# Optimization experiments

Measured on AMD Instinct MI355X. Metric: run time of the kernel, lower is better.

Reference implementation:

```python
import jax, jax.numpy as jnp
import numpy as np

N = 8192
E = 262144
D_IN = 768
D_STRUCT = 32
D_HID = 768
D_OUT = 768
MEM_K = 64
MEM_D = 768
NUM_GRAPHS = 64


def setup_inputs() -> dict:
    key = jax.random.key(0)
    ks = jax.random.split(key, 16)
    s = 0.02
    return {
        "feature": jax.random.normal(ks[0], (N, D_IN), jnp.float32),
        "ppr": jax.random.uniform(ks[1], (N,), jnp.float32),
        "edge_attr": jax.random.normal(ks[2], (E, D_IN), jnp.float32),
        "Ws": jax.random.normal(ks[3], (1, D_STRUCT), jnp.float32) * s,
        "bs": jnp.zeros((D_STRUCT,), jnp.float32),
        "W1": jax.random.normal(ks[4], (D_IN + D_STRUCT, D_HID), jnp.float32) * s,
        "b1": jnp.zeros((D_HID,), jnp.float32),
        "prelu_a": jnp.asarray(0.25, jnp.float32),
        "W2": jax.random.normal(ks[5], (D_HID, D_OUT), jnp.float32) * s,
        "b2": jnp.zeros((D_OUT,), jnp.float32),
        "Wp1": jax.random.normal(ks[6], (D_HID, D_HID), jnp.float32) * s,
        "bp1": jnp.zeros((D_HID,), jnp.float32),
        "Wp2": jax.random.normal(ks[7], (D_HID, D_OUT), jnp.float32) * s,
        "bp2": jnp.zeros((D_OUT,), jnp.float32),
        "memory": jax.random.normal(ks[8], (MEM_K, MEM_D), jnp.float32),
        "edge_index": jax.random.randint(ks[9], (2, E), 0, N, jnp.int64),
        "batch_ids": jnp.sort(jax.random.randint(ks[10], (N,), 0, NUM_GRAPHS, jnp.int64)),
        "num_graphs": NUM_GRAPHS,
    }


def reference(feature, ppr, edge_attr, Ws, bs, W1, b1, prelu_a, W2, b2,
              Wp1, bp1, Wp2, bp2, memory, edge_index, batch_ids, num_graphs):
    n = feature.shape[0]
    # aggre_edges: scatter_add edge_attr onto destination nodes (col)
    col = edge_index[1]
    feat = feature + jax.ops.segment_sum(edge_attr, col, num_segments=n)
    # struct encoder: Linear(1, struct_dim) + ReLU on ppr scalar
    struct_feat = jax.nn.relu(ppr[:, None] @ Ws + bs)  # [N, 32]
    # MLP: Linear -> PReLU -> Linear
    h = jnp.concatenate([feat, struct_feat], axis=-1) @ W1 + b1
    h = jnp.where(h > 0, h, prelu_a * h)
    node_feats = h @ W2 + b2  # [N, D_OUT]
    # scatter_mean over graphs
    seg_sum = jax.ops.segment_sum(node_feats, batch_ids, num_segments=num_graphs)
    cnt = jax.ops.segment_sum(jnp.ones((n,), node_feats.dtype), batch_ids, num_segments=num_graphs)
    graph_feats = seg_sum / jnp.maximum(cnt, 1.0)[:, None]
    pooled_feats = jnp.tanh(graph_feats @ Wp1 + bp1) @ Wp2 + bp2
    # memory attention: softmax(M @ nf) over memory slots, then mean(mem_key * M)
    # mean_k(softmax(scores)[n,k] * M[k,d]) == (softmax @ M) / K
    w = jax.nn.softmax(node_feats @ memory.T, axis=1)  # [N, 64]
    re_node_feats = (w @ memory) / memory.shape[0]      # [N, 768]
    loss = jnp.mean((node_feats - re_node_feats) ** 2)
    return pooled_feats, re_node_feats, loss
```

## Files before the change

kernel.cpp:

```cpp
#include <hip/hip_runtime.h>
#include <hip/hip_bf16.h>
#include <math.h>

typedef unsigned short ushort_t;
typedef short bf16x8 __attribute__((ext_vector_type(8)));
typedef float f32x4 __attribute__((ext_vector_type(4)));

#define NNODES   8192
#define DIN      768
#define DSTRUCT  32
#define XDIM     800
#define DHID     768
#define DOUT     768
#define MEMK     64
#define NGRAPH   64
#define BUCKET_CAP 128

#define OFF_XHI     0u
#define OFF_XLO     (OFF_XHI  + 8192u*800u*2u)
#define OFF_HHI     (OFF_XLO  + 8192u*800u*2u)
#define OFF_HLO     (OFF_HHI  + 8192u*768u*2u)
#define OFF_NF      (OFF_HLO  + 8192u*768u*2u)
#define OFF_NFHI    (OFF_NF   + 8192u*768u*4u)
#define OFF_NFLO    (OFF_NFHI + 8192u*768u*2u)
#define OFF_W1THI   (OFF_NFLO + 8192u*768u*2u)
#define OFF_W1TLO   (OFF_W1THI + 768u*800u*2u)
#define OFF_W2THI   (OFF_W1TLO + 768u*800u*2u)
#define OFF_W2TLO   (OFF_W2THI + 768u*768u*2u)
#define OFF_MHI     (OFF_W2TLO + 768u*768u*2u)
#define OFF_MLO     (OFF_MHI  + 64u*768u*2u)
#define OFF_MTHI    (OFF_MLO  + 64u*768u*2u)
#define OFF_MTLO    (OFF_MTHI + 768u*64u*2u)
#define OFF_BUCKET  (OFF_MTLO + 768u*64u*2u)
#define OFF_COUNTS  (OFF_BUCKET + 8192u*BUCKET_CAP*4u)
#define OFF_GSTART  (OFF_COUNTS + 8192u*4u)
#define OFF_GEND    (OFF_GSTART + 256u)
#define OFF_LOSS    (OFF_GEND + 256u)
#define OFF_GFEAT   (OFF_LOSS + 256u)
#define OFF_T1      (OFF_GFEAT + 768u*64u*4u)
#define ZERO_OFF    OFF_COUNTS
#define ZERO_BYTES  (8192u*4u + 256u + 256u + 256u)

__device__ __forceinline__ ushort_t bf_rne(float f) {
    unsigned u = __float_as_uint(f);
    return (ushort_t)((u + 0x7FFFu + ((u >> 16) & 1u)) >> 16);
}
__device__ __forceinline__ void split_bf16(float f, ushort_t& hi, ushort_t& lo) {
    ushort_t h = bf_rne(f);
    float fh = __uint_as_float(((unsigned)h) << 16);
    hi = h;
    lo = bf_rne(f - fh);
}
__device__ __forceinline__ void gld16(const void* g, void* l) {
    __builtin_amdgcn_global_load_lds(
        (const __attribute__((address_space(1))) unsigned int*)g,
        (__attribute__((address_space(3))) unsigned int*)l, 16, 0, 0);
}

__global__ void k_fill_bucket(const int* __restrict__ col, int* __restrict__ counts,
                              int* __restrict__ bucket, int E) {
    for (int e = blockIdx.x * blockDim.x + threadIdx.x; e < E; e += gridDim.x * blockDim.x) {
        int c = col[e];
        if ((unsigned)c < (unsigned)NNODES) {
            int p = atomicAdd(&counts[c], 1);
            if (p < BUCKET_CAP) bucket[c * BUCKET_CAP + p] = e;
        }
    }
}

__global__ __launch_bounds__(192) void k_aggregate(
    const float* __restrict__ feature, const float* __restrict__ edge_attr,
    const float* __restrict__ ppr, const float* __restrict__ Ws, const float* __restrict__ bs,
    const int* __restrict__ bucket, const int* __restrict__ counts,
    ushort_t* __restrict__ Xhi, ushort_t* __restrict__ Xlo) {
    int n = blockIdx.x;
    int t = threadIdx.x;
    const float4* frow = (const float4*)(feature + (size_t)n * DIN);
    float4 acc = frow[t];
    int deg = min(counts[n], BUCKET_CAP);
    const int* bk = bucket + n * BUCKET_CAP;
    for (int j = 0; j < deg; ++j) {
        int e = bk[j];
        float4 v = ((const float4*)(edge_attr + (size_t)e * DIN))[t];
        acc.x += v.x; acc.y += v.y; acc.z += v.z; acc.w += v.w;
    }
    ushort4 h4, l4;
    split_bf16(acc.x, h4.x, l4.x); split_bf16(acc.y, h4.y, l4.y);
    split_bf16(acc.z, h4.z, l4.z); split_bf16(acc.w, h4.w, l4.w);
    *(ushort4*)(Xhi + (size_t)n * XDIM + t * 4) = h4;
    *(ushort4*)(Xlo + (size_t)n * XDIM + t * 4) = l4;
    if (t < DSTRUCT / 4) {
        float p = ppr[n];
        int k = t * 4;
        float4 s;
        s.x = fmaxf(p * Ws[k+0] + bs[k+0], 0.f);
        s.y = fmaxf(p * Ws[k+1] + bs[k+1], 0.f);
        s.z = fmaxf(p * Ws[k+2] + bs[k+2], 0.f);
        s.w = fmaxf(p * Ws[k+3] + bs[k+3], 0.f);
        ushort4 sh, sl;
        split_bf16(s.x, sh.x, sl.x); split_bf16(s.y, sh.y, sl.y);
        split_bf16(s.z, sh.z, sl.z); split_bf16(s.w, sh.w, sl.w);
        *(ushort4*)(Xhi + (size_t)n * XDIM + DIN + k) = sh;
        *(ushort4*)(Xlo + (size_t)n * XDIM + DIN + k) = sl;
    }
}

__global__ __launch_bounds__(256) void k_wsplit(const float* __restrict__ W,
                                                ushort_t* __restrict__ Thi, ushort_t* __restrict__ Tlo,
                                                int K, int N) {
    __shared__ float tile[32][33];
    int n0 = blockIdx.x * 32, k0 = blockIdx.y * 32;
    int tx = threadIdx.x & 31, ty = threadIdx.x >> 5;
#pragma unroll
    for (int i = 0; i < 4; ++i) {
        int k = ty + i * 8;
        tile[k][tx] = W[(size_t)(k0 + k) * N + n0 + tx];
    }
    __syncthreads();
#pragma unroll
    for (int i = 0; i < 4; ++i) {
        int nn = ty + i * 8;
        float v = tile[tx][nn];
        ushort_t hi, lo; split_bf16(v, hi, lo);
        Thi[(size_t)(n0 + nn) * K + k0 + tx] = hi;
        Tlo[(size_t)(n0 + nn) * K + k0 + tx] = lo;
    }
}

__global__ void k_msplit(const float* __restrict__ m, ushort_t* __restrict__ hi,
                         ushort_t* __restrict__ lo, int n) {
    int i = blockIdx.x * 256 + threadIdx.x;
    if (i >= n) return;
    ushort_t h, l; split_bf16(m[i], h, l);
    hi[i] = h; lo[i] = l;
}

#define L_ALO 2048
#define L_BHI 4096
#define L_BLO 8192
#define L_BUF 12288

template<int ACT, int OUTMODE>
__global__ __launch_bounds__(256) void k_gemm_mfma(
    const ushort_t* __restrict__ Ahi, const ushort_t* __restrict__ Alo,
    const ushort_t* __restrict__ Bhi, const ushort_t* __restrict__ Blo,
    const float* __restrict__ bias, const float* __restrict__ act_p,
    float* __restrict__ Cf, ushort_t* __restrict__ Chi, ushort_t* __restrict__ Clo,
    int M, int N, int K) {
    __shared__ ushort_t lds[2 * L_BUF];
    int tid = threadIdx.x;
    int l = tid & 63, w = tid >> 6;

    int nbx = N / 128;
    int nwg = nbx * (M / 64);
    int bid = blockIdx.y * nbx + blockIdx.x;
    int q = nwg >> 3;
    int nb = (bid & 7) * q + (bid >> 3);
    int bx = nb % nbx, by = nb / nbx;
    int m0 = by * 64, n0 = bx * 128;

    int wm = w >> 1, wn = w & 1;

    f32x4 acc[2][4];
#pragma unroll
    for (int m = 0; m < 2; ++m)
#pragma unroll
        for (int n = 0; n < 4; ++n) acc[m][n] = (f32x4){0.f, 0.f, 0.f, 0.f};

    int srow = w * 16 + (l >> 2);
    int sc   = (l & 3) * 8;
    const ushort_t* agh  = Ahi + (size_t)(m0 + srow) * K + sc;
    const ushort_t* agl  = Alo + (size_t)(m0 + srow) * K + sc;
    const ushort_t* bgh0 = Bhi + (size_t)(n0 + srow) * K + sc;
    const ushort_t* bgh1 = Bhi + (size_t)(n0 + 64 + srow) * K + sc;
    const ushort_t* bgl0 = Blo + (size_t)(n0 + srow) * K + sc;
    const ushort_t* bgl1 = Blo + (size_t)(n0 + 64 + srow) * K + sc;

    int NT = K / 32;

    {
        ushort_t* b = lds;
        gld16(agh,  b + w * 512);
        gld16(agl,  b + L_ALO + w * 512);
        gld16(bgh0, b + L_BHI + w * 512);
        gld16(bgh1, b + L_BHI + 2048 + w * 512);
        gld16(bgl0, b + L_BLO + w * 512);
        gld16(bgl1, b + L_BLO + 2048 + w * 512);
    }

    int c0 = l >> 4;
    int arow = wm * 32 + (l & 15);
    int bcol = wn * 64 + (l & 15);

    for (int kt = 0; kt < NT; ++kt) {
        int cur = kt & 1;
        __syncthreads();
        if (kt + 1 < NT) {
            int ko = (kt + 1) * 32;
            ushort_t* b = lds + (cur ^ 1) * L_BUF;
            gld16(agh + ko,  b + w * 512);
            gld16(agl + ko,  b + L_ALO + w * 512);
            gld16(bgh0 + ko, b + L_BHI + w * 512);
            gld16(bgh1 + ko, b + L_BHI + 2048 + w * 512);
            gld16(bgl0 + ko, b + L_BLO + w * 512);
            gld16(bgl1 + ko, b + L_BLO + 2048 + w * 512);
        }
        const ushort_t* cb = lds + cur * L_BUF;
        bf16x8 ah[2], al[2], bh[4], bl[4];
#pragma unroll
        for (int m = 0; m < 2; ++m) {
            ah[m] = *(const bf16x8*)(cb + (arow + m * 16) * 32 + c0 * 8);
            al[m] = *(const bf16x8*)(cb + L_ALO + (arow + m * 16) * 32 + c0 * 8);
        }
#pragma unroll
        for (int n = 0; n < 4; ++n) {
            bh[n] = *(const bf16x8*)(cb + L_BHI + (bcol + n * 16) * 32 + c0 * 8);
            bl[n] = *(const bf16x8*)(cb + L_BLO + (bcol + n * 16) * 32 + c0 * 8);
        }
#pragma unroll
        for (int m = 0; m < 2; ++m)
#pragma unroll
            for (int n = 0; n < 4; ++n) {
                acc[m][n] = __builtin_amdgcn_mfma_f32_16x16x32_bf16(ah[m], bh[n], acc[m][n], 0, 0, 0);
                acc[m][n] = __builtin_amdgcn_mfma_f32_16x16x32_bf16(ah[m], bl[n], acc[m][n], 0, 0, 0);
                acc[m][n] = __builtin_amdgcn_mfma_f32_16x16x32_bf16(al[m], bh[n], acc[m][n], 0, 0, 0);
            }
    }

    float ap = (ACT == 1) ? *act_p : 0.f;
#pragma unroll
    for (int m = 0; m < 2; ++m)
#pragma unroll
        for (int n = 0; n < 4; ++n) {
            int col = n0 + wn * 64 + n * 16 + (l & 15);
            float bv = bias[col];
#pragma unroll
            for (int r = 0; r < 4; ++r) {
                int row = m0 + wm * 32 + m * 16 + (l >> 4) * 4 + r;
                float x = acc[m][n][r] + bv;
                if (ACT == 1) x = x > 0.f ? x : ap * x;
                ushort_t hi, lo; split_bf16(x, hi, lo);
                Chi[(size_t)row * N + col] = hi;
                Clo[(size_t)row * N + col] = lo;
                if (OUTMODE == 2) Cf[(size_t)row * N + col] = x;
            }
        }
}

__global__ void k_boundaries(const int* __restrict__ batch, int* __restrict__ gstart,
                             int* __restrict__ gend, int n) {
    int i = blockIdx.x * blockDim.x + threadIdx.x;
    if (i >= n) return;
    int b = batch[i];
    if ((unsigned)b >= (unsigned)NGRAPH) return;
    if (i == 0 || batch[i - 1] != b) gstart[b] = i;
    if (i == n - 1 || batch[i + 1] != b) gend[b] = i + 1;
}

__global__ __launch_bounds__(128) void k_pool(const float* __restrict__ nf,
                                              const int* __restrict__ gstart, const int* __restrict__ gend,
                                              float* __restrict__ gfeatT) {
    int g = blockIdx.x, d = blockIdx.y * 128 + threadIdx.x;
    int s = gstart[g], e = gend[g];
    float a = 0.f;
    for (int n = s; n < e; ++n) a += nf[(size_t)n * DOUT + d];
    gfeatT[(size_t)d * 64 + g] = a / fmaxf((float)(e - s), 1.f);
}

template<int ACT>
__global__ __launch_bounds__(256) void k_mlp_t(const float* __restrict__ AT, const float* __restrict__ B,
                                               const float* __restrict__ bias,
                                               float* __restrict__ OutT, float* __restrict__ OutR) {
    __shared__ float red[4][64];
    int n = blockIdx.x;
    int l = threadIdx.x & 63, qw = threadIdx.x >> 6;
    float s = 0.f;
    const float* a = AT + l;
    const float* b = B + n;
#pragma unroll 8
    for (int k = qw * 192; k < qw * 192 + 192; ++k)
        s = fmaf(a[k * 64], b[k * 768], s);
    red[qw][l] = s;
    __syncthreads();
    if (threadIdx.x < 64) {
        float v = red[0][l] + red[1][l] + red[2][l] + red[3][l] + bias[n];
        if (ACT == 2) { v = tanhf(v); OutT[n * 64 + l] = v; }
        else OutR[(size_t)l * 768 + n] = v;
    }
}

__global__ __launch_bounds__(256) void k_attn(
    const ushort_t* __restrict__ NFhi, const ushort_t* __restrict__ NFlo,
    const ushort_t* __restrict__ Mhi,  const ushort_t* __restrict__ Mlo,
    const ushort_t* __restrict__ MThi, const ushort_t* __restrict__ MTlo,
    const float* __restrict__ nf, float* __restrict__ re, float* __restrict__ lossac) {
    __shared__ ushort_t Ah[96 * 32 * 8];
    __shared__ ushort_t Al[96 * 32 * 8];
    __shared__ ushort_t Wp[2][32 * 64];
    __shared__ float xch[4][32];
    __shared__ float lred[4];
    int tid = threadIdx.x, l = tid & 63, w = tid >> 6;
    int g = l >> 4, li = l & 15;
    int base = blockIdx.x * 32;

    for (int i = w * 12; i < w * 12 + 12; ++i) {
        int kc = i * 2 + (l >> 5), row = l & 31;
        gld16(NFhi + (size_t)(base + row) * 768 + kc * 8, Ah + i * 512);
        gld16(NFlo + (size_t)(base + row) * 768 + kc * 8, Al + i * 512);
    }
    __syncthreads();

    f32x4 sacc[2];
    sacc[0] = (f32x4){0.f,0.f,0.f,0.f}; sacc[1] = (f32x4){0.f,0.f,0.f,0.f};
    int slot = w * 16 + li;
#pragma unroll 4
    for (int kt = 0; kt < 24; ++kt) {
        bf16x8 ah0 = *(const bf16x8*)(Ah + (kt * 4 + g) * 256 + li * 8);
        bf16x8 ah1 = *(const bf16x8*)(Ah + (kt * 4 + g) * 256 + (li + 16) * 8);
        bf16x8 al0 = *(const bf16x8*)(Al + (kt * 4 + g) * 256 + li * 8);
        bf16x8 al1 = *(const bf16x8*)(Al + (kt * 4 + g) * 256 + (li + 16) * 8);
        bf16x8 bh  = *(const bf16x8*)(Mhi + (size_t)slot * 768 + kt * 32 + g * 8);
        bf16x8 bl  = *(const bf16x8*)(Mlo + (size_t)slot * 768 + kt * 32 + g * 8);
        sacc[0] = __builtin_amdgcn_mfma_f32_16x16x32_bf16(ah0, bh, sacc[0], 0, 0, 0);
        sacc[0] = __builtin_amdgcn_mfma_f32_16x16x32_bf16(ah0, bl, sacc[0], 0, 0, 0);
        sacc[0] = __builtin_amdgcn_mfma_f32_16x16x32_bf16(al0, bh, sacc[0], 0, 0, 0);
        sacc[1] = __builtin_amdgcn_mfma_f32_16x16x32_bf16(ah1, bh, sacc[1], 0, 0, 0);
        sacc[1] = __builtin_amdgcn_mfma_f32_16x16x32_bf16(ah1, bl, sacc[1], 0, 0, 0);
        sacc[1] = __builtin_amdgcn_mfma_f32_16x16x32_bf16(al1, bh, sacc[1], 0, 0, 0);
    }

    float mxv[8];
#pragma unroll
    for (int m = 0; m < 2; ++m)
#pragma unroll
        for (int r = 0; r < 4; ++r) {
            float v = sacc[m][r];
            v = fmaxf(v, __shfl_xor(v, 1)); v = fmaxf(v, __shfl_xor(v, 2));
            v = fmaxf(v, __shfl_xor(v, 4)); v = fmaxf(v, __shfl_xor(v, 8));
            mxv[m * 4 + r] = v;
        }
    if (li == 0) {
#pragma unroll
        for (int m = 0; m < 2; ++m)
#pragma unroll
            for (int r = 0; r < 4; ++r) xch[w][m * 16 + g * 4 + r] = mxv[m * 4 + r];
    }
    __syncthreads();
    float ev[8], sv[8];
#pragma unroll
    for (int m = 0; m < 2; ++m)
#pragma unroll
        for (int r = 0; r < 4; ++r) {
            int row = m * 16 + g * 4 + r;
            float mx = fmaxf(fmaxf(xch[0][row], xch[1][row]), fmaxf(xch[2][row], xch[3][row]));
            float e = __expf(sacc[m][r] - mx);
            ev[m * 4 + r] = e;
            float s = e;
            s += __shfl_xor(s, 1); s += __shfl_xor(s, 2);
            s += __shfl_xor(s, 4); s += __shfl_xor(s, 8);
            sv[m * 4 + r] = s;
        }
    __syncthreads();
    if (li == 0) {
#pragma unroll
        for (int m = 0; m < 2; ++m)
#pragma unroll
            for (int r = 0; r < 4; ++r) xch[w][m * 16 + g * 4 + r] = sv[m * 4 + r];
    }
    __syncthreads();
#pragma unroll
    for (int m = 0; m < 2; ++m)
#pragma unroll
        for (int r = 0; r < 4; ++r) {
            int row = m * 16 + g * 4 + r;
            float tot = xch[0][row] + xch[1][row] + xch[2][row] + xch[3][row];
            float wv = ev[m * 4 + r] / tot;
            ushort_t hi, lo; split_bf16(wv, hi, lo);
            int idx = row * 64 + (slot ^ ((row & 7) << 3));
            Wp[0][idx] = hi; Wp[1][idx] = lo;
        }
    __syncthreads();

    bf16x8 wah[2][2], wal[2][2];
#pragma unroll
    for (int m = 0; m < 2; ++m)
#pragma unroll
        for (int kt2 = 0; kt2 < 2; ++kt2) {
            int row = m * 16 + li;
            int k8 = kt2 * 4 + g;
            int idx = row * 64 + ((k8 * 8) ^ ((row & 7) << 3));
            wah[m][kt2] = *(const bf16x8*)&Wp[0][idx];
            wal[m][kt2] = *(const bf16x8*)&Wp[1][idx];
        }
    float lp = 0.f;
#pragma unroll 2
    for (int nfi = 0; nfi < 12; ++nfi) {
        int col = w * 192 + nfi * 16 + li;
        f32x4 pacc[2];
        pacc[0] = (f32x4){0.f,0.f,0.f,0.f}; pacc[1] = (f32x4){0.f,0.f,0.f,0.f};
#pragma unroll
        for (int kt2 = 0; kt2 < 2; ++kt2) {
            bf16x8 bh = *(const bf16x8*)(MThi + (size_t)col * 64 + kt2 * 32 + g * 8);
            bf16x8 bl = *(const bf16x8*)(MTlo + (size_t)col * 64 + kt2 * 32 + g * 8);
#pragma unroll
            for (int m = 0; m < 2; ++m) {
                pacc[m] = __builtin_amdgcn_mfma_f32_16x16x32_bf16(wah[m][kt2], bh, pacc[m], 0, 0, 0);
                pacc[m] = __builtin_amdgcn_mfma_f32_16x16x32_bf16(wah[m][kt2], bl, pacc[m], 0, 0, 0);
                pacc[m] = __builtin_amdgcn_mfma_f32_16x16x32_bf16(wal[m][kt2], bh, pacc[m], 0, 0, 0);
            }
        }
#pragma unroll
        for (int m = 0; m < 2; ++m)
#pragma unroll
            for (int r = 0; r < 4; ++r) {
                int row = base + m * 16 + g * 4 + r;
                float v = pacc[m][r] * (1.f / 64.f);
                float x = nf[(size_t)row * 768 + col];
                re[(size_t)row * 768 + col] = v;
                float d = x - v;
                lp = fmaf(d, d, lp);
            }
    }
    for (int o = 32; o; o >>= 1) lp += __shfl_xor(lp, o);
    if (l == 0) lred[w] = lp;
    __syncthreads();
    if (tid == 0) atomicAdd(lossac, lred[0] + lred[1] + lred[2] + lred[3]);
}

__global__ void k_loss_final(const float* __restrict__ acc, float* __restrict__ out, float invn) {
    if (threadIdx.x == 0 && blockIdx.x == 0) out[0] = acc[0] * invn;
}

extern "C" void kernel_launch(void* const* d_in, const int* in_sizes, int n_in,
                              void* d_out, int out_size, void* d_ws, size_t ws_size,
                              hipStream_t stream) {
    const float* feature  = (const float*)d_in[0];
    const float* ppr      = (const float*)d_in[1];
    const float* edge_attr= (const float*)d_in[2];
    const float* Ws       = (const float*)d_in[3];
    const float* bs       = (const float*)d_in[4];
    const float* W1       = (const float*)d_in[5];
    const float* b1       = (const float*)d_in[6];
    const float* prelu_a  = (const float*)d_in[7];
    const float* W2       = (const float*)d_in[8];
    const float* b2       = (const float*)d_in[9];
    const float* Wp1      = (const float*)d_in[10];
    const float* bp1      = (const float*)d_in[11];
    const float* Wp2      = (const float*)d_in[12];
    const float* bp2      = (const float*)d_in[13];
    const float* memory   = (const float*)d_in[14];
    const int*   edge_index = (const int*)d_in[15];
    const int*   batch_ids  = (const int*)d_in[16];

    const int E = in_sizes[15] / 2;
    const int N = in_sizes[0] / DIN;
    const int* col = edge_index + E;

    char* ws = (char*)d_ws;
    ushort_t* Xhi  = (ushort_t*)(ws + OFF_XHI);
    ushort_t* Xlo  = (ushort_t*)(ws + OFF_XLO);
    ushort_t* Hhi  = (ushort_t*)(ws + OFF_HHI);
    ushort_t* Hlo  = (ushort_t*)(ws + OFF_HLO);
    float*    nf   = (float*)   (ws + OFF_NF);
    ushort_t* NFhi = (ushort_t*)(ws + OFF_NFHI);
    ushort_t* NFlo = (ushort_t*)(ws + OFF_NFLO);
    ushort_t* W1Thi= (ushort_t*)(ws + OFF_W1THI);
    ushort_t* W1Tlo= (ushort_t*)(ws + OFF_W1TLO);
    ushort_t* W2Thi= (ushort_t*)(ws + OFF_W2THI);
    ushort_t* W2Tlo= (ushort_t*)(ws + OFF_W2TLO);
    ushort_t* Mhi  = (ushort_t*)(ws + OFF_MHI);
    ushort_t* Mlo  = (ushort_t*)(ws + OFF_MLO);
    ushort_t* MThi = (ushort_t*)(ws + OFF_MTHI);
    ushort_t* MTlo = (ushort_t*)(ws + OFF_MTLO);
    int*   bucket = (int*)(ws + OFF_BUCKET);
    int*   counts = (int*)(ws + OFF_COUNTS);
    int*   gstart = (int*)(ws + OFF_GSTART);
    int*   gend   = (int*)(ws + OFF_GEND);
    float* lossac = (float*)(ws + OFF_LOSS);
    float* gfeatT = (float*)(ws + OFF_GFEAT);
    float* t1T    = (float*)(ws + OFF_T1);

    float* out_pooled = (float*)d_out;
    float* out_re     = (float*)d_out + NGRAPH * DOUT;
    float* out_loss   = (float*)d_out + NGRAPH * DOUT + (size_t)N * DOUT;

    (void)hipMemsetAsync(ws + ZERO_OFF, 0, ZERO_BYTES, stream);

    k_wsplit<<<dim3(768 / 32, 800 / 32), 256, 0, stream>>>(W1, W1Thi, W1Tlo, XDIM, DHID);
    k_wsplit<<<dim3(768 / 32, 768 / 32), 256, 0, stream>>>(W2, W2Thi, W2Tlo, DHID, DOUT);
    k_wsplit<<<dim3(768 / 32, 64 / 32), 256, 0, stream>>>(memory, MThi, MTlo, MEMK, DOUT);
    k_msplit<<<(MEMK * 768 + 255) / 256, 256, 0, stream>>>(memory, Mhi, Mlo, MEMK * 768);

    k_fill_bucket<<<1024, 256, 0, stream>>>(col, counts, bucket, E);
    k_aggregate<<<N, 192, 0, stream>>>(feature, edge_attr, ppr, Ws, bs, bucket, counts, Xhi, Xlo);

    k_gemm_mfma<1, 1><<<dim3(DHID / 128, N / 64), 256, 0, stream>>>(
        Xhi, Xlo, W1Thi, W1Tlo, b1, prelu_a, nullptr, Hhi, Hlo, N, DHID, XDIM);
    k_gemm_mfma<0, 2><<<dim3(DOUT / 128, N / 64), 256, 0, stream>>>(
        Hhi, Hlo, W2Thi, W2Tlo, b2, nullptr, nf, NFhi, NFlo, N, DOUT, DHID);

    k_boundaries<<<(N + 255) / 256, 256, 0, stream>>>(batch_ids, gstart, gend, N);
    k_pool<<<dim3(NGRAPH, 6), 128, 0, stream>>>(nf, gstart, gend, gfeatT);

    k_mlp_t<2><<<768, 256, 0, stream>>>(gfeatT, Wp1, bp1, t1T, nullptr);
    k_mlp_t<0><<<768, 256, 0, stream>>>(t1T, Wp2, bp2, nullptr, out_pooled);

    k_attn<<<N / 32, 256, 0, stream>>>(NFhi, NFlo, Mhi, Mlo, MThi, MTlo, nf, out_re, lossac);
    k_loss_final<<<1, 64, 0, stream>>>(lossac, out_loss, 1.f / (float)((size_t)N * DOUT));
}
```

Measured before the change: 414.4 us.

## Drop fp32 node-feature buffer and reorganize GEMM LDS tile layout

Removes the fp32 copy of node features written by the second GEMM; the pooling and attention kernels now rebuild each value from its bf16 hi/lo pair. This cuts about 25 MB of global writes and the matching reads. The GEMM's global-to-LDS staging is also remapped so each 16-row block is stored k-chunk-major. That makes the per-lane bf16x8 LDS reads contiguous across lanes and should reduce bank conflicts. The rebuilt value differs slightly from the original fp32 (about 16 mantissa bits), which changes the loss and pooling numerics a little.

```diff
diff --git a/kernel.cpp b/kernel.cpp
--- a/kernel.cpp
+++ b/kernel.cpp
@@ -20,8 +20,7 @@
 #define OFF_XLO     (OFF_XHI  + 8192u*800u*2u)
 #define OFF_HHI     (OFF_XLO  + 8192u*800u*2u)
 #define OFF_HLO     (OFF_HHI  + 8192u*768u*2u)
-#define OFF_NF      (OFF_HLO  + 8192u*768u*2u)
-#define OFF_NFHI    (OFF_NF   + 8192u*768u*4u)
+#define OFF_NFHI    (OFF_HLO  + 8192u*768u*2u)
 #define OFF_NFLO    (OFF_NFHI + 8192u*768u*2u)
 #define OFF_W1THI   (OFF_NFLO + 8192u*768u*2u)
 #define OFF_W1TLO   (OFF_W1THI + 768u*800u*2u)
@@ -51,6 +50,9 @@
     hi = h;
     lo = bf_rne(f - fh);
 }
+__device__ __forceinline__ float join_bf16(ushort_t hi, ushort_t lo) {
+    return __uint_as_float(((unsigned)hi) << 16) + __uint_as_float(((unsigned)lo) << 16);
+}
 __device__ __forceinline__ void gld16(const void* g, void* l) {
     __builtin_amdgcn_global_load_lds(
         (const __attribute__((address_space(1))) unsigned int*)g,
@@ -140,12 +142,12 @@
 #define L_BLO 8192
 #define L_BUF 12288
 
-template<int ACT, int OUTMODE>
+template<int ACT>
 __global__ __launch_bounds__(256) void k_gemm_mfma(
     const ushort_t* __restrict__ Ahi, const ushort_t* __restrict__ Alo,
     const ushort_t* __restrict__ Bhi, const ushort_t* __restrict__ Blo,
     const float* __restrict__ bias, const float* __restrict__ act_p,
-    float* __restrict__ Cf, ushort_t* __restrict__ Chi, ushort_t* __restrict__ Clo,
+    ushort_t* __restrict__ Chi, ushort_t* __restrict__ Clo,
     int M, int N, int K) {
     __shared__ ushort_t lds[2 * L_BUF];
     int tid = threadIdx.x;
@@ -167,8 +169,8 @@
 #pragma unroll
         for (int n = 0; n < 4; ++n) acc[m][n] = (f32x4){0.f, 0.f, 0.f, 0.f};
 
-    int srow = w * 16 + (l >> 2);
-    int sc   = (l & 3) * 8;
+    int srow = w * 16 + (l & 15);
+    int sc   = (l >> 4) * 8;
     const ushort_t* agh  = Ahi + (size_t)(m0 + srow) * K + sc;
     const ushort_t* agl  = Alo + (size_t)(m0 + srow) * K + sc;
     const ushort_t* bgh0 = Bhi + (size_t)(n0 + srow) * K + sc;
@@ -189,8 +191,7 @@
     }
 
     int c0 = l >> 4;
-    int arow = wm * 32 + (l & 15);
-    int bcol = wn * 64 + (l & 15);
+    int li = l & 15;
 
     for (int kt = 0; kt < NT; ++kt) {
         int cur = kt & 1;
@@ -209,13 +210,13 @@
         bf16x8 ah[2], al[2], bh[4], bl[4];
 #pragma unroll
         for (int m = 0; m < 2; ++m) {
-            ah[m] = *(const bf16x8*)(cb + (arow + m * 16) * 32 + c0 * 8);
-            al[m] = *(const bf16x8*)(cb + L_ALO + (arow + m * 16) * 32 + c0 * 8);
+            ah[m] = *(const bf16x8*)(cb + (wm * 2 + m) * 512 + c0 * 128 + li * 8);
+            al[m] = *(const bf16x8*)(cb + L_ALO + (wm * 2 + m) * 512 + c0 * 128 + li * 8);
         }
 #pragma unroll
         for (int n = 0; n < 4; ++n) {
-            bh[n] = *(const bf16x8*)(cb + L_BHI + (bcol + n * 16) * 32 + c0 * 8);
-            bl[n] = *(const bf16x8*)(cb + L_BLO + (bcol + n * 16) * 32 + c0 * 8);
+            bh[n] = *(const bf16x8*)(cb + L_BHI + (wn * 4 + n) * 512 + c0 * 128 + li * 8);
+            bl[n] = *(const bf16x8*)(cb + L_BLO + (wn * 4 + n) * 512 + c0 * 128 + li * 8);
         }
 #pragma unroll
         for (int m = 0; m < 2; ++m)
@@ -242,7 +243,6 @@
                 ushort_t hi, lo; split_bf16(x, hi, lo);
                 Chi[(size_t)row * N + col] = hi;
                 Clo[(size_t)row * N + col] = lo;
-                if (OUTMODE == 2) Cf[(size_t)row * N + col] = x;
             }
         }
 }
@@ -257,13 +257,15 @@
     if (i == n - 1 || batch[i + 1] != b) gend[b] = i + 1;
 }
 
-__global__ __launch_bounds__(128) void k_pool(const float* __restrict__ nf,
+__global__ __launch_bounds__(128) void k_pool(const ushort_t* __restrict__ NFhi,
+                                              const ushort_t* __restrict__ NFlo,
                                               const int* __restrict__ gstart, const int* __restrict__ gend,
                                               float* __restrict__ gfeatT) {
     int g = blockIdx.x, d = blockIdx.y * 128 + threadIdx.x;
     int s = gstart[g], e = gend[g];
     float a = 0.f;
-    for (int n = s; n < e; ++n) a += nf[(size_t)n * DOUT + d];
+    for (int n = s; n < e; ++n)
+        a += join_bf16(NFhi[(size_t)n * DOUT + d], NFlo[(size_t)n * DOUT + d]);
     gfeatT[(size_t)d * 64 + g] = a / fmaxf((float)(e - s), 1.f);
 }
 
@@ -293,7 +295,7 @@
     const ushort_t* __restrict__ NFhi, const ushort_t* __restrict__ NFlo,
     const ushort_t* __restrict__ Mhi,  const ushort_t* __restrict__ Mlo,
     const ushort_t* __restrict__ MThi, const ushort_t* __restrict__ MTlo,
-    const float* __restrict__ nf, float* __restrict__ re, float* __restrict__ lossac) {
+    float* __restrict__ re, float* __restrict__ lossac) {
     __shared__ ushort_t Ah[96 * 32 * 8];
     __shared__ ushort_t Al[96 * 32 * 8];
     __shared__ ushort_t Wp[2][32 * 64];
@@ -415,7 +417,7 @@
             for (int r = 0; r < 4; ++r) {
                 int row = base + m * 16 + g * 4 + r;
                 float v = pacc[m][r] * (1.f / 64.f);
-                float x = nf[(size_t)row * 768 + col];
+                float x = join_bf16(NFhi[(size_t)row * 768 + col], NFlo[(size_t)row * 768 + col]);
                 re[(size_t)row * 768 + col] = v;
                 float d = x - v;
                 lp = fmaf(d, d, lp);
@@ -461,7 +463,6 @@
     ushort_t* Xlo  = (ushort_t*)(ws + OFF_XLO);
     ushort_t* Hhi  = (ushort_t*)(ws + OFF_HHI);
     ushort_t* Hlo  = (ushort_t*)(ws + OFF_HLO);
-    float*    nf   = (float*)   (ws + OFF_NF);
     ushort_t* NFhi = (ushort_t*)(ws + OFF_NFHI);
     ushort_t* NFlo = (ushort_t*)(ws + OFF_NFLO);
     ushort_t* W1Thi= (ushort_t*)(ws + OFF_W1THI);
@@ -494,17 +495,17 @@
     k_fill_bucket<<<1024, 256, 0, stream>>>(col, counts, bucket, E);
     k_aggregate<<<N, 192, 0, stream>>>(feature, edge_attr, ppr, Ws, bs, bucket, counts, Xhi, Xlo);
 
-    k_gemm_mfma<1, 1><<<dim3(DHID / 128, N / 64), 256, 0, stream>>>(
-        Xhi, Xlo, W1Thi, W1Tlo, b1, prelu_a, nullptr, Hhi, Hlo, N, DHID, XDIM);
-    k_gemm_mfma<0, 2><<<dim3(DOUT / 128, N / 64), 256, 0, stream>>>(
-        Hhi, Hlo, W2Thi, W2Tlo, b2, nullptr, nf, NFhi, NFlo, N, DOUT, DHID);
+    k_gemm_mfma<1><<<dim3(DHID / 128, N / 64), 256, 0, stream>>>(
+        Xhi, Xlo, W1Thi, W1Tlo, b1, prelu_a, Hhi, Hlo, N, DHID, XDIM);
+    k_gemm_mfma<0><<<dim3(DOUT / 128, N / 64), 256, 0, stream>>>(
+        Hhi, Hlo, W2Thi, W2Tlo, b2, nullptr, NFhi, NFlo, N, DOUT, DHID);
 
     k_boundaries<<<(N + 255) / 256, 256, 0, stream>>>(batch_ids, gstart, gend, N);
-    k_pool<<<dim3(NGRAPH, 6), 128, 0, stream>>>(nf, gstart, gend, gfeatT);
+    k_pool<<<dim3(NGRAPH, 6), 128, 0, stream>>>(NFhi, NFlo, gstart, gend, gfeatT);
 
     k_mlp_t<2><<<768, 256, 0, stream>>>(gfeatT, Wp1, bp1, t1T, nullptr);
     k_mlp_t<0><<<768, 256, 0, stream>>>(t1T, Wp2, bp2, nullptr, out_pooled);
 
-    k_attn<<<N / 32, 256, 0, stream>>>(NFhi, NFlo, Mhi, Mlo, MThi, MTlo, nf, out_re, lossac);
+    k_attn<<<N / 32, 256, 0, stream>>>(NFhi, NFlo, Mhi, Mlo, MThi, MTlo, out_re, lossac);
     k_loss_final<<<1, 64, 0, stream>>>(lossac, out_loss, 1.f / (float)((size_t)N * DOUT));
 }
```

Measured after the change: 439.5 us. 6.0% more time.
